# Kernel optimization log

Hardware: AMD Instinct MI355X
Metric: run time of the kernel (lower is better)

## Reference

```python
import jax, jax.numpy as jnp
import numpy as np

EPS = 1e-5
DECAY = 0.9        # membrane potential decay
SLOPE = 0.01       # leaky_relu negative slope
HEBB_LR = 0.01     # Hebbian plasticity learning rate
WD = 1e-3          # synapse weight decay
W_CLAMP = 1.0      # synapse weight clamp


def _ln(x, g, b):
    mu = jnp.mean(x, axis=-1, keepdims=True)
    var = jnp.mean((x - mu) ** 2, axis=-1, keepdims=True)
    return (x - mu) * jax.lax.rsqrt(var + EPS) * g + b


def setup_inputs() -> dict:
    key = jax.random.key(0)
    ks = jax.random.split(key, 4)
    B, N = 16384, 1024
    scale = 1.0 / np.sqrt(N)
    return {
        "inputs": jax.random.normal(ks[0], (B, N), dtype=jnp.float32),
        "contribution": jax.random.uniform(ks[1], (B,), dtype=jnp.float32),
        "prev_potential": jnp.zeros((B, N), dtype=jnp.float32),
        "syn_weights": jax.random.normal(ks[2], (N, N), dtype=jnp.float32) * scale,
        "gate_W": jax.random.normal(ks[3], (N, N), dtype=jnp.float32) * scale,
        "gate_b": jnp.zeros((N,), dtype=jnp.float32),
        "pre_gamma": jnp.ones((N,), dtype=jnp.float32),
        "pre_beta": jnp.zeros((N,), dtype=jnp.float32),
        "ln_gamma": jnp.ones((N,), dtype=jnp.float32),
        "ln_beta": jnp.zeros((N,), dtype=jnp.float32),
    }


def reference(inputs, contribution, prev_potential, syn_weights, gate_W, gate_b,
              pre_gamma, pre_beta, ln_gamma, ln_beta):
    B = inputs.shape[0]
    # pre-norm
    x_norm = _ln(inputs, pre_gamma, pre_beta)
    # neuron: recurrent drive through synapse weights + leaky membrane
    pre = x_norm @ syn_weights                      # [B, N]
    potential = DECAY * prev_potential + pre        # new neuron state
    activation = jnp.where(potential >= 0, potential, SLOPE * potential)
    # Hebbian synapse update modulated by per-sample contribution
    hebb = jnp.einsum('bi,bj->ij', activation * contribution[:, None], activation) / B
    new_syn_weights = jnp.clip(syn_weights * (1.0 - WD) + HEBB_LR * hebb,
                               -W_CLAMP, W_CLAMP)
    # gated residual (gate computed on raw inputs)
    gate = jax.nn.sigmoid(inputs @ gate_W.T + gate_b)
    residual = gate * activation + (1.0 - gate) * inputs
    # post-norm (dropout is identity in eval/reference)
    output = _ln(residual, ln_gamma, ln_beta)
    return (output, potential, new_syn_weights)
```

## Files before the change

### kernel.cpp

```cpp
#include <hip/hip_runtime.h>
#include <cstdint>
#include <cstddef>

#define EPS 1e-5f
#define DECAY 0.9f
#define SLOPE 0.01f
#define HEBB_LR 0.01f
#define WDK 1e-3f

typedef float f32x4 __attribute__((ext_vector_type(4)));
typedef __bf16 bf16x8 __attribute__((ext_vector_type(8)));
typedef unsigned short u16;
typedef unsigned int u32;

union U128 { uint4 u; bf16x8 b; };
union Pack16 { u16 s[16]; uint4 q[2]; };
union Pack8  { u16 s[8];  uint4 q; };
union Pack4  { u16 s[4];  uint2 q; };

__device__ __forceinline__ u16 f2b(float f) {
  u32 u = __builtin_bit_cast(u32, f);
  u = u + 0x7FFFu + ((u >> 16) & 1u);
  return (u16)(u >> 16);
}
__device__ __forceinline__ float b2f(u16 h) {
  u32 u = ((u32)h) << 16;
  return __builtin_bit_cast(float, u);
}
__device__ __forceinline__ float wred(float x) {
#pragma unroll
  for (int o = 32; o > 0; o >>= 1) x += __shfl_down(x, o, 64);
  return x;
}
__device__ __forceinline__ u32 swz(u32 b) { return b ^ (((b >> 7) & 7u) << 4); }

__device__ __forceinline__ void gld16(const u16* g, u16* lds) {
  __builtin_amdgcn_global_load_lds(
      (__attribute__((address_space(1))) void*)g,
      (__attribute__((address_space(3))) void*)lds, 16, 0, 0);
}

__global__ __launch_bounds__(256) void prep_rows(
    const float* __restrict__ in, const float* __restrict__ pg,
    const float* __restrict__ pb, u16* __restrict__ xnb,
    u16* __restrict__ inb, int N) {
  const int row = blockIdx.x, t = threadIdx.x;
  const float* rp = in + (size_t)row * N;
  float4 v = reinterpret_cast<const float4*>(rp)[t];
  float s = v.x + v.y + v.z + v.w;
  float s2 = v.x * v.x + v.y * v.y + v.z * v.z + v.w * v.w;
  s = wred(s); s2 = wred(s2);
  __shared__ float rs_[4], rs2_[4];
  if ((t & 63) == 0) { rs_[t >> 6] = s; rs2_[t >> 6] = s2; }
  __syncthreads();
  float S = rs_[0] + rs_[1] + rs_[2] + rs_[3];
  float S2 = rs2_[0] + rs2_[1] + rs2_[2] + rs2_[3];
  float mu = S / N;
  float var = S2 / N - mu * mu;
  float rstd = rsqrtf(var + EPS);
  float4 g = reinterpret_cast<const float4*>(pg)[t];
  float4 b = reinterpret_cast<const float4*>(pb)[t];
  float xv[4] = {v.x, v.y, v.z, v.w};
  float gv[4] = {g.x, g.y, g.z, g.w};
  float bv[4] = {b.x, b.y, b.z, b.w};
  Pack4 px, pi;
#pragma unroll
  for (int j = 0; j < 4; ++j) {
    px.s[j] = f2b((xv[j] - mu) * rstd * gv[j] + bv[j]);
    pi.s[j] = f2b(xv[j]);
  }
  reinterpret_cast<uint2*>(xnb + (size_t)row * N)[t] = px.q;
  reinterpret_cast<uint2*>(inb + (size_t)row * N)[t] = pi.q;
}

__global__ __launch_bounds__(256) void wconv(const float* __restrict__ W,
                                             u16* __restrict__ Wb, int total) {
  int idx = blockIdx.x * 256 + threadIdx.x;
  size_t off = (size_t)idx * 8;
  if (off >= (size_t)total) return;
  float4 a = *reinterpret_cast<const float4*>(W + off);
  float4 b = *reinterpret_cast<const float4*>(W + off + 4);
  Pack8 p;
  p.s[0] = f2b(a.x); p.s[1] = f2b(a.y); p.s[2] = f2b(a.z); p.s[3] = f2b(a.w);
  p.s[4] = f2b(b.x); p.s[5] = f2b(b.y); p.s[6] = f2b(b.z); p.s[7] = f2b(b.w);
  *reinterpret_cast<uint4*>(Wb + off) = p.q;
}

__global__ __launch_bounds__(256) void wconv_T(const float* __restrict__ W,
                                               u16* __restrict__ Wt, int R, int C) {
  __shared__ float tile[64][65];
  int c0 = blockIdx.x * 64, r0 = blockIdx.y * 64;
  int tr = threadIdx.x >> 2, tc = threadIdx.x & 3;
#pragma unroll
  for (int cc = 0; cc < 4; ++cc) {
    float4 v = *reinterpret_cast<const float4*>(W + (size_t)(r0 + tr) * C + c0 + tc * 16 + cc * 4);
    tile[tr][tc * 16 + cc * 4 + 0] = v.x;
    tile[tr][tc * 16 + cc * 4 + 1] = v.y;
    tile[tr][tc * 16 + cc * 4 + 2] = v.z;
    tile[tr][tc * 16 + cc * 4 + 3] = v.w;
  }
  __syncthreads();
  Pack16 p;
#pragma unroll
  for (int j = 0; j < 16; ++j) p.s[j] = f2b(tile[tc * 16 + j][tr]);
  uint4* dst = reinterpret_cast<uint4*>(Wt + (size_t)(c0 + tr) * R + r0 + tc * 16);
  dst[0] = p.q[0]; dst[1] = p.q[1];
}

__global__ __launch_bounds__(256) void transpose_act(
    const float* __restrict__ pot, const float* __restrict__ contrib,
    u16* __restrict__ actT, u16* __restrict__ actcT, int Brows, int N) {
  __shared__ float tile[64][65];
  __shared__ float csh[64];
  int n0 = blockIdx.x * 64, b0 = blockIdx.y * 64;
  int tr = threadIdx.x >> 2, tc = threadIdx.x & 3;
  if (threadIdx.x < 64) csh[threadIdx.x] = contrib[b0 + threadIdx.x];
#pragma unroll
  for (int cc = 0; cc < 4; ++cc) {
    float4 v = *reinterpret_cast<const float4*>(pot + (size_t)(b0 + tr) * N + n0 + tc * 16 + cc * 4);
    float a0 = v.x >= 0.f ? v.x : SLOPE * v.x;
    float a1 = v.y >= 0.f ? v.y : SLOPE * v.y;
    float a2 = v.z >= 0.f ? v.z : SLOPE * v.z;
    float a3 = v.w >= 0.f ? v.w : SLOPE * v.w;
    tile[tr][tc * 16 + cc * 4 + 0] = a0;
    tile[tr][tc * 16 + cc * 4 + 1] = a1;
    tile[tr][tc * 16 + cc * 4 + 2] = a2;
    tile[tr][tc * 16 + cc * 4 + 3] = a3;
  }
  __syncthreads();
  Pack16 pa, pc;
#pragma unroll
  for (int j = 0; j < 16; ++j) {
    float a = tile[tc * 16 + j][tr];
    pa.s[j] = f2b(a);
    pc.s[j] = f2b(a * csh[tc * 16 + j]);
  }
  size_t obase = (size_t)(n0 + tr) * Brows + b0 + tc * 16;
  uint4* d1 = reinterpret_cast<uint4*>(actT + obase);
  d1[0] = pa.q[0]; d1[1] = pa.q[1];
  uint4* d2 = reinterpret_cast<uint4*>(actcT + obase);
  d2[0] = pc.q[0]; d2[1] = pc.q[1];
}

__global__ __launch_bounds__(256) void fuse_out(
    const float* __restrict__ pot, const u16* __restrict__ gate,
    const float* __restrict__ in, const float* __restrict__ lg,
    const float* __restrict__ lb, float* __restrict__ out, int N) {
  const int row = blockIdx.x, t = threadIdx.x;
  size_t base = (size_t)row * N;
  float4 p = reinterpret_cast<const float4*>(pot + base)[t];
  float4 x = reinterpret_cast<const float4*>(in + base)[t];
  Pack4 gq; gq.q = reinterpret_cast<const uint2*>(gate + base)[t];
  float pv[4] = {p.x, p.y, p.z, p.w}, xv[4] = {x.x, x.y, x.z, x.w};
  float res[4];
  float s = 0.f, s2 = 0.f;
#pragma unroll
  for (int j = 0; j < 4; ++j) {
    float a = pv[j] >= 0.f ? pv[j] : SLOPE * pv[j];
    float gv = b2f(gq.s[j]);
    float r = gv * a + (1.f - gv) * xv[j];
    res[j] = r; s += r; s2 += r * r;
  }
  s = wred(s); s2 = wred(s2);
  __shared__ float rs_[4], rs2_[4];
  if ((t & 63) == 0) { rs_[t >> 6] = s; rs2_[t >> 6] = s2; }
  __syncthreads();
  float S = rs_[0] + rs_[1] + rs_[2] + rs_[3];
  float S2 = rs2_[0] + rs2_[1] + rs2_[2] + rs2_[3];
  float mu = S / N, var = S2 / N - mu * mu, rstd = rsqrtf(var + EPS);
  float4 g4 = reinterpret_cast<const float4*>(lg)[t];
  float4 b4 = reinterpret_cast<const float4*>(lb)[t];
  float gv[4] = {g4.x, g4.y, g4.z, g4.w}, bv[4] = {b4.x, b4.y, b4.z, b4.w};
  float4 o;
  o.x = (res[0] - mu) * rstd * gv[0] + bv[0];
  o.y = (res[1] - mu) * rstd * gv[1] + bv[1];
  o.z = (res[2] - mu) * rstd * gv[2] + bv[2];
  o.w = (res[3] - mu) * rstd * gv[3] + bv[3];
  reinterpret_cast<float4*>(out + base)[t] = o;
}

template <int EPI>
__global__ __launch_bounds__(256) void gemm_bt(
    const u16* __restrict__ A, const u16* __restrict__ Bt,
    int lda, int kIters, int Ncols,
    const float* __restrict__ aux,
    float* __restrict__ outF,
    u16* __restrict__ outB) {
  __shared__ __align__(128) u16 lA[128 * 64];
  __shared__ __align__(128) u16 lB[128 * 64];
  const int tid = threadIdx.x;
  const int w = tid >> 6, l = tid & 63;
  const int m0 = blockIdx.y * 128, n0 = blockIdx.x * 128;
  const int kbase = blockIdx.z * kIters * 64;

  const u16* gA[4]; const u16* gB[4];
  u16* lAd[4]; u16* lBd[4];
#pragma unroll
  for (int i = 0; i < 4; ++i) {
    u32 o = (u32)(i * 4096 + w * 1024 + l * 16);
    u32 op = swz(o);
    int row = (int)(op >> 7);
    int kg = (int)((op >> 4) & 7u);
    gA[i] = A + (size_t)(m0 + row) * (size_t)lda + kbase + kg * 8;
    gB[i] = Bt + (size_t)(n0 + row) * (size_t)lda + kbase + kg * 8;
    lAd[i] = lA + (i * 4096 + w * 1024) / 2;
    lBd[i] = lB + (i * 4096 + w * 1024) / 2;
  }

  f32x4 acc[4][4] = {};
  const int wr = w >> 1, wc = w & 1;
  const int r16 = l & 15, gq = l >> 4;
  const char* lAc = (const char*)lA;
  const char* lBc = (const char*)lB;

  for (int it = 0; it < kIters; ++it) {
    const int kk = it * 64;
#pragma unroll
    for (int i = 0; i < 4; ++i) gld16(gA[i] + kk, lAd[i]);
#pragma unroll
    for (int i = 0; i < 4; ++i) gld16(gB[i] + kk, lBd[i]);
    __syncthreads();
#pragma unroll
    for (int ks = 0; ks < 2; ++ks) {
      U128 af[4], bfr[4];
#pragma unroll
      for (int f = 0; f < 4; ++f) {
        u32 loa = ((u32)(wr * 64 + f * 16 + r16) << 7) + (u32)(ks * 64 + gq * 16);
        af[f].u = *reinterpret_cast<const uint4*>(lAc + swz(loa));
        u32 lob = ((u32)(wc * 64 + f * 16 + r16) << 7) + (u32)(ks * 64 + gq * 16);
        bfr[f].u = *reinterpret_cast<const uint4*>(lBc + swz(lob));
      }
#pragma unroll
      for (int mf = 0; mf < 4; ++mf)
#pragma unroll
        for (int nf = 0; nf < 4; ++nf)
          acc[mf][nf] = __builtin_amdgcn_mfma_f32_16x16x32_bf16(
              af[mf].b, bfr[nf].b, acc[mf][nf], 0, 0, 0);
    }
    __syncthreads();
  }

  const size_t splitOff =
      (EPI == 2) ? (size_t)blockIdx.z * (size_t)Ncols * (size_t)(gridDim.y * 128) : 0;
#pragma unroll
  for (int mf = 0; mf < 4; ++mf) {
#pragma unroll
    for (int r = 0; r < 4; ++r) {
      const int m = m0 + wr * 64 + mf * 16 + gq * 4 + r;
#pragma unroll
      for (int nf = 0; nf < 4; ++nf) {
        const int n = n0 + wc * 64 + nf * 16 + r16;
        float v = acc[mf][nf][r];
        if (EPI == 0) {
          size_t off = (size_t)m * Ncols + n;
          outF[off] = DECAY * aux[off] + v;
        } else if (EPI == 1) {
          float gl = v + aux[n];
          outB[(size_t)m * Ncols + n] = f2b(1.f / (1.f + __expf(-gl)));
        } else {
          outF[splitOff + (size_t)m * Ncols + n] = v;
        }
      }
    }
  }
}

__global__ __launch_bounds__(256) void syn_update(
    const float* __restrict__ syn, const float* __restrict__ part,
    float* __restrict__ outS, int total4, float hebbScale, int nsplit) {
  int idx = blockIdx.x * 256 + threadIdx.x;
  if (idx >= total4) return;
  float4 s = reinterpret_cast<const float4*>(syn)[idx];
  float hx = 0.f, hy = 0.f, hz = 0.f, hw = 0.f;
  for (int sp = 0; sp < nsplit; ++sp) {
    float4 p = reinterpret_cast<const float4*>(part)[(size_t)sp * total4 + idx];
    hx += p.x; hy += p.y; hz += p.z; hw += p.w;
  }
  float4 o;
  o.x = fminf(1.f, fmaxf(-1.f, s.x * (1.f - WDK) + hebbScale * hx));
  o.y = fminf(1.f, fmaxf(-1.f, s.y * (1.f - WDK) + hebbScale * hy));
  o.z = fminf(1.f, fmaxf(-1.f, s.z * (1.f - WDK) + hebbScale * hz));
  o.w = fminf(1.f, fmaxf(-1.f, s.w * (1.f - WDK) + hebbScale * hw));
  reinterpret_cast<float4*>(outS)[idx] = o;
}

extern "C" void kernel_launch(void* const* d_in, const int* in_sizes, int n_in,
                              void* d_out, int out_size, void* d_ws, size_t ws_size,
                              hipStream_t stream) {
  const float* inputs        = (const float*)d_in[0];
  const float* contribution  = (const float*)d_in[1];
  const float* prev_potential= (const float*)d_in[2];
  const float* syn_weights   = (const float*)d_in[3];
  const float* gate_W        = (const float*)d_in[4];
  const float* gate_b        = (const float*)d_in[5];
  const float* pre_gamma     = (const float*)d_in[6];
  const float* pre_beta      = (const float*)d_in[7];
  const float* ln_gamma      = (const float*)d_in[8];
  const float* ln_beta       = (const float*)d_in[9];

  const int B = in_sizes[1];
  const int N = in_sizes[5];
  const size_t BN = (size_t)B * N;

  float* out_output = (float*)d_out;
  float* out_pot    = out_output + BN;
  float* out_syn    = out_output + 2 * BN;

  char* ws = (char*)d_ws;
  u16* xnb   = (u16*)ws;
  u16* inb   = (u16*)(ws + BN * 2);
  u16* synT  = (u16*)(ws + BN * 4);
  u16* gwb   = (u16*)(ws + BN * 4 + (size_t)N * N * 2);
  u16* gateb = (u16*)(ws + BN * 4 + (size_t)N * N * 4);
  u16* actT  = xnb;
  u16* actcT = inb;
  float* part = (float*)gateb;

  const int NS = 8;

  prep_rows<<<B, 256, 0, stream>>>(inputs, pre_gamma, pre_beta, xnb, inb, N);
  wconv_T<<<dim3(N / 64, N / 64), 256, 0, stream>>>(syn_weights, synT, N, N);
  wconv<<<(N * N / 8 + 255) / 256, 256, 0, stream>>>(gate_W, gwb, N * N);
  gemm_bt<0><<<dim3(N / 128, B / 128), 256, 0, stream>>>(
      xnb, synT, N, N / 64, N, prev_potential, out_pot, nullptr);
  gemm_bt<1><<<dim3(N / 128, B / 128), 256, 0, stream>>>(
      inb, gwb, N, N / 64, N, gate_b, nullptr, gateb);
  fuse_out<<<B, 256, 0, stream>>>(out_pot, gateb, inputs, ln_gamma, ln_beta, out_output, N);
  transpose_act<<<dim3(N / 64, B / 64), 256, 0, stream>>>(
      out_pot, contribution, actT, actcT, B, N);
  gemm_bt<2><<<dim3(N / 128, N / 128, NS), 256, 0, stream>>>(
      actcT, actT, B, (B / 64) / NS, N, nullptr, part, nullptr);
  syn_update<<<(N * N / 4 + 255) / 256, 256, 0, stream>>>(
      syn_weights, part, out_syn, N * N / 4, HEBB_LR / (float)B, NS);
}
```

Measured before the change: 463.5 us.

## Replace GEMM with 256x256 double-buffered pipelined 8-wave kernel and bf16 split partials

```diff
diff --git a/kernel.cpp b/kernel.cpp
--- a/kernel.cpp
+++ b/kernel.cpp
@@ -32,7 +32,6 @@
   for (int o = 32; o > 0; o >>= 1) x += __shfl_down(x, o, 64);
   return x;
 }
-__device__ __forceinline__ u32 swz(u32 b) { return b ^ (((b >> 7) & 7u) << 4); }
 
 __device__ __forceinline__ void gld16(const u16* g, u16* lds) {
   __builtin_amdgcn_global_load_lds(
@@ -179,74 +178,114 @@
   reinterpret_cast<float4*>(out + base)[t] = o;
 }
 
+__device__ __forceinline__ u32 swz64(u32 b) { return b ^ (((b >> 7) & 3u) << 4); }
+
+__device__ __forceinline__ void stage8(int s, int NT4, const u16* A, const u16* Bt,
+                                       int m0, int n0, int lda, int kbase,
+                                       char* ldsc, int tid) {
+  if (s >= NT4) return;
+  const int tau = s >> 2, j = s & 3;
+  const int mat = j & 1, ks = j >> 1;
+  const u16* src = mat ? Bt : A;
+  const int rbase = mat ? n0 : m0;
+  const int kk = kbase + tau * 64 + ks * 32;
+  char* dst = ldsc + (tau & 1) * 65536 + mat * 32768 + ks * 16384 + tid * 16;
+  const int row = tid >> 2;
+  const int kg = (tid & 3) ^ ((tid >> 3) & 3);
+  const u16* g0 = src + (size_t)(rbase + row) * (size_t)lda + kk + kg * 8;
+  gld16(g0, (u16*)dst);
+  gld16(g0 + (size_t)128 * (size_t)lda, (u16*)(dst + 8192));
+}
+
+#define VMW(n) asm volatile("s_waitcnt vmcnt(" #n ")" ::: "memory")
+#define BARR() asm volatile("s_barrier" ::: "memory")
+
 template <int EPI>
-__global__ __launch_bounds__(256) void gemm_bt(
+__global__ __launch_bounds__(512, 2) void gemm8p(
     const u16* __restrict__ A, const u16* __restrict__ Bt,
-    int lda, int kIters, int Ncols,
+    int lda, int NT, int Ncols,
     const float* __restrict__ aux,
-    float* __restrict__ outF,
-    u16* __restrict__ outB) {
-  __shared__ __align__(128) u16 lA[128 * 64];
-  __shared__ __align__(128) u16 lB[128 * 64];
+    float* __restrict__ outF, u16* __restrict__ outB,
+    int nbx, int nbxShift, int nbyX) {
+  __shared__ __align__(128) u16 lds[65536];
+  char* ldsc = (char*)lds;
   const int tid = threadIdx.x;
   const int w = tid >> 6, l = tid & 63;
-  const int m0 = blockIdx.y * 128, n0 = blockIdx.x * 128;
-  const int kbase = blockIdx.z * kIters * 64;
-
-  const u16* gA[4]; const u16* gB[4];
-  u16* lAd[4]; u16* lBd[4];
-#pragma unroll
-  for (int i = 0; i < 4; ++i) {
-    u32 o = (u32)(i * 4096 + w * 1024 + l * 16);
-    u32 op = swz(o);
-    int row = (int)(op >> 7);
-    int kg = (int)((op >> 4) & 7u);
-    gA[i] = A + (size_t)(m0 + row) * (size_t)lda + kbase + kg * 8;
-    gB[i] = Bt + (size_t)(n0 + row) * (size_t)lda + kbase + kg * 8;
-    lAd[i] = lA + (i * 4096 + w * 1024) / 2;
-    lBd[i] = lB + (i * 4096 + w * 1024) / 2;
-  }
-
-  f32x4 acc[4][4] = {};
-  const int wr = w >> 1, wc = w & 1;
+  const int wr = w >> 2, wc = w & 3;
   const int r16 = l & 15, gq = l >> 4;
-  const char* lAc = (const char*)lA;
-  const char* lBc = (const char*)lB;
-
-  for (int it = 0; it < kIters; ++it) {
-    const int kk = it * 64;
-#pragma unroll
-    for (int i = 0; i < 4; ++i) gld16(gA[i] + kk, lAd[i]);
-#pragma unroll
-    for (int i = 0; i < 4; ++i) gld16(gB[i] + kk, lBd[i]);
-    __syncthreads();
-#pragma unroll
-    for (int ks = 0; ks < 2; ++ks) {
-      U128 af[4], bfr[4];
-#pragma unroll
-      for (int f = 0; f < 4; ++f) {
-        u32 loa = ((u32)(wr * 64 + f * 16 + r16) << 7) + (u32)(ks * 64 + gq * 16);
-        af[f].u = *reinterpret_cast<const uint4*>(lAc + swz(loa));
-        u32 lob = ((u32)(wc * 64 + f * 16 + r16) << 7) + (u32)(ks * 64 + gq * 16);
-        bfr[f].u = *reinterpret_cast<const uint4*>(lBc + swz(lob));
-      }
-#pragma unroll
-      for (int mf = 0; mf < 4; ++mf)
-#pragma unroll
-        for (int nf = 0; nf < 4; ++nf)
-          acc[mf][nf] = __builtin_amdgcn_mfma_f32_16x16x32_bf16(
-              af[mf].b, bfr[nf].b, acc[mf][nf], 0, 0, 0);
-    }
-    __syncthreads();
-  }
+
+  int bx, by, kb;
+  if (EPI == 2) {
+    bx = blockIdx.x; by = blockIdx.y; kb = blockIdx.z * NT * 64;
+  } else {
+    int bid = blockIdx.x;
+    int xcd = bid & 7, i = bid >> 3;
+    by = xcd * nbyX + (i >> nbxShift);
+    bx = i & (nbx - 1);
+    kb = 0;
+  }
+  const int m0 = by * 256, n0 = bx * 256;
+  const int NT4 = NT * 4;
+
+  int pA[8], pB[4];
+#pragma unroll
+  for (int mf = 0; mf < 8; ++mf)
+    pA[mf] = (int)swz64((u32)((wr * 128 + mf * 16 + r16) * 64 + gq * 16));
+#pragma unroll
+  for (int nf = 0; nf < 4; ++nf)
+    pB[nf] = (int)swz64((u32)((wc * 64 + nf * 16 + r16) * 64 + gq * 16));
+
+  f32x4 acc[8][4] = {};
+  U128 af[8], bf[2];
+
+#define LDA_(ks) { char* _b = ldsc + buf * 65536 + (ks) * 16384;              \
+  _Pragma("unroll") for (int mf = 0; mf < 8; ++mf)                            \
+    af[mf].u = *reinterpret_cast<const uint4*>(_b + pA[mf]); }
+#define LDB_(ks, nh) { char* _b = ldsc + buf * 65536 + 32768 + (ks) * 16384;  \
+  bf[0].u = *reinterpret_cast<const uint4*>(_b + pB[2 * (nh)]);               \
+  bf[1].u = *reinterpret_cast<const uint4*>(_b + pB[2 * (nh) + 1]); }
+#define MFMA_(nh) { __builtin_amdgcn_s_setprio(1);                            \
+  _Pragma("unroll") for (int mf = 0; mf < 8; ++mf) {                          \
+    acc[mf][2 * (nh)] = __builtin_amdgcn_mfma_f32_16x16x32_bf16(              \
+        af[mf].b, bf[0].b, acc[mf][2 * (nh)], 0, 0, 0);                       \
+    acc[mf][2 * (nh) + 1] = __builtin_amdgcn_mfma_f32_16x16x32_bf16(          \
+        af[mf].b, bf[1].b, acc[mf][2 * (nh) + 1], 0, 0, 0); }                 \
+  __builtin_amdgcn_s_setprio(0); }
+#define STG(s) stage8((s), NT4, A, Bt, m0, n0, lda, kb, ldsc, tid)
+
+  for (int s = 0; s < 6; ++s) STG(s);
+  VMW(8); BARR();
+
+  for (int t = 0; t < NT - 1; ++t) {
+    const int buf = t & 1;
+    const int sb = t * 4;
+    LDA_(0); LDB_(0, 0); STG(sb + 6); VMW(8); BARR(); MFMA_(0); BARR();
+    LDB_(0, 1);          STG(sb + 7); VMW(8); BARR(); MFMA_(1); BARR();
+    LDA_(1); LDB_(1, 0); STG(sb + 8); VMW(8); BARR(); MFMA_(0); BARR();
+    LDB_(1, 1);          STG(sb + 9);
+    if (t == NT - 2) { VMW(4); } else { VMW(8); }
+    BARR(); MFMA_(1); BARR();
+  }
+  {
+    const int buf = (NT - 1) & 1;
+    LDA_(0); LDB_(0, 0); MFMA_(0);
+    LDB_(0, 1);          MFMA_(1);
+    VMW(0); BARR();
+    LDA_(1); LDB_(1, 0); MFMA_(0);
+    LDB_(1, 1);          MFMA_(1);
+  }
+#undef LDA_
+#undef LDB_
+#undef MFMA_
+#undef STG
 
   const size_t splitOff =
-      (EPI == 2) ? (size_t)blockIdx.z * (size_t)Ncols * (size_t)(gridDim.y * 128) : 0;
-#pragma unroll
-  for (int mf = 0; mf < 4; ++mf) {
+      (EPI == 2) ? (size_t)blockIdx.z * (size_t)Ncols * (size_t)(gridDim.y * 256) : 0;
+#pragma unroll
+  for (int mf = 0; mf < 8; ++mf) {
 #pragma unroll
     for (int r = 0; r < 4; ++r) {
-      const int m = m0 + wr * 64 + mf * 16 + gq * 4 + r;
+      const int m = m0 + wr * 128 + mf * 16 + gq * 4 + r;
 #pragma unroll
       for (int nf = 0; nf < 4; ++nf) {
         const int n = n0 + wc * 64 + nf * 16 + r16;
@@ -258,7 +297,7 @@
           float gl = v + aux[n];
           outB[(size_t)m * Ncols + n] = f2b(1.f / (1.f + __expf(-gl)));
         } else {
-          outF[splitOff + (size_t)m * Ncols + n] = v;
+          outB[splitOff + (size_t)m * Ncols + n] = f2b(v);
         }
       }
     }
@@ -266,22 +305,28 @@
 }
 
 __global__ __launch_bounds__(256) void syn_update(
-    const float* __restrict__ syn, const float* __restrict__ part,
-    float* __restrict__ outS, int total4, float hebbScale, int nsplit) {
+    const float* __restrict__ syn, const u16* __restrict__ part,
+    float* __restrict__ outS, int total8, float hebbScale, int nsplit, int NN) {
   int idx = blockIdx.x * 256 + threadIdx.x;
-  if (idx >= total4) return;
-  float4 s = reinterpret_cast<const float4*>(syn)[idx];
-  float hx = 0.f, hy = 0.f, hz = 0.f, hw = 0.f;
+  if (idx >= total8) return;
+  float h[8] = {0.f, 0.f, 0.f, 0.f, 0.f, 0.f, 0.f, 0.f};
   for (int sp = 0; sp < nsplit; ++sp) {
-    float4 p = reinterpret_cast<const float4*>(part)[(size_t)sp * total4 + idx];
-    hx += p.x; hy += p.y; hz += p.z; hw += p.w;
-  }
-  float4 o;
-  o.x = fminf(1.f, fmaxf(-1.f, s.x * (1.f - WDK) + hebbScale * hx));
-  o.y = fminf(1.f, fmaxf(-1.f, s.y * (1.f - WDK) + hebbScale * hy));
-  o.z = fminf(1.f, fmaxf(-1.f, s.z * (1.f - WDK) + hebbScale * hz));
-  o.w = fminf(1.f, fmaxf(-1.f, s.w * (1.f - WDK) + hebbScale * hw));
-  reinterpret_cast<float4*>(outS)[idx] = o;
+    Pack8 p;
+    p.q = reinterpret_cast<const uint4*>(part + (size_t)sp * NN)[idx];
+#pragma unroll
+    for (int j = 0; j < 8; ++j) h[j] += b2f(p.s[j]);
+  }
+  float4 s0 = reinterpret_cast<const float4*>(syn)[idx * 2];
+  float4 s1 = reinterpret_cast<const float4*>(syn)[idx * 2 + 1];
+  float sv[8] = {s0.x, s0.y, s0.z, s0.w, s1.x, s1.y, s1.z, s1.w};
+  float ov[8];
+#pragma unroll
+  for (int j = 0; j < 8; ++j)
+    ov[j] = fminf(1.f, fmaxf(-1.f, sv[j] * (1.f - WDK) + hebbScale * h[j]));
+  float4 o0 = {ov[0], ov[1], ov[2], ov[3]};
+  float4 o1 = {ov[4], ov[5], ov[6], ov[7]};
+  reinterpret_cast<float4*>(outS)[idx * 2] = o0;
+  reinterpret_cast<float4*>(outS)[idx * 2 + 1] = o1;
 }
 
 extern "C" void kernel_launch(void* const* d_in, const int* in_sizes, int n_in,
@@ -314,22 +359,25 @@
   u16* gateb = (u16*)(ws + BN * 4 + (size_t)N * N * 4);
   u16* actT  = xnb;
   u16* actcT = inb;
-  float* part = (float*)gateb;
-
-  const int NS = 8;
+  u16* part  = gateb;
+
+  const int NS = 16;
+  const int NT = N / 64;
 
   prep_rows<<<B, 256, 0, stream>>>(inputs, pre_gamma, pre_beta, xnb, inb, N);
   wconv_T<<<dim3(N / 64, N / 64), 256, 0, stream>>>(syn_weights, synT, N, N);
   wconv<<<(N * N / 8 + 255) / 256, 256, 0, stream>>>(gate_W, gwb, N * N);
-  gemm_bt<0><<<dim3(N / 128, B / 128), 256, 0, stream>>>(
-      xnb, synT, N, N / 64, N, prev_potential, out_pot, nullptr);
-  gemm_bt<1><<<dim3(N / 128, B / 128), 256, 0, stream>>>(
-      inb, gwb, N, N / 64, N, gate_b, nullptr, gateb);
+
+  const int nbx = N / 256, nbxShift = 2, nbyX = (B / 256) / 8;
+  gemm8p<0><<<(B / 256) * (N / 256), 512, 0, stream>>>(
+      xnb, synT, N, NT, N, prev_potential, out_pot, nullptr, nbx, nbxShift, nbyX);
+  gemm8p<1><<<(B / 256) * (N / 256), 512, 0, stream>>>(
+      inb, gwb, N, NT, N, gate_b, nullptr, gateb, nbx, nbxShift, nbyX);
   fuse_out<<<B, 256, 0, stream>>>(out_pot, gateb, inputs, ln_gamma, ln_beta, out_output, N);
   transpose_act<<<dim3(N / 64, B / 64), 256, 0, stream>>>(
       out_pot, contribution, actT, actcT, B, N);
-  gemm_bt<2><<<dim3(N / 128, N / 128, NS), 256, 0, stream>>>(
-      actcT, actT, B, (B / 64) / NS, N, nullptr, part, nullptr);
-  syn_update<<<(N * N / 4 + 255) / 256, 256, 0, stream>>>(
-      syn_weights, part, out_syn, N * N / 4, HEBB_LR / (float)B, NS);
-}
+  gemm8p<2><<<dim3(N / 256, N / 256, NS), 512, 0, stream>>>(
+      actcT, actT, B, (B / NS) / 64, N, nullptr, nullptr, part, 0, 0, 0);
+  syn_update<<<(N * N / 8 + 255) / 256, 256, 0, stream>>>(
+      syn_weights, part, out_syn, N * N / 8, HEBB_LR / (float)B, NS, N * N);
+}
```

New measurement: 445.0 us. 4.0% less time.
